# Kernel optimization log

Measured on AMD Instinct MI355X. Metric: run time of the kernel, lower is better.

Reference implementation:

```python
import jax, jax.numpy as jnp
import numpy as np

B, S, D, H = 4, 2048, 512, 8  # batch, seq, input_dim=feature_dim, n_heads


def setup_inputs() -> dict:
    key = jax.random.key(0)
    ks = jax.random.split(key, 12)
    s = 1.0 / np.sqrt(D)
    return {
        "q": jax.random.normal(ks[0], (B, S, D), jnp.float32),
        "k": jax.random.normal(ks[1], (B, S, D), jnp.float32),
        "v": jax.random.normal(ks[2], (B, S, D), jnp.float32),
        "mask": jax.random.randint(ks[3], (B, S), 0, 2, jnp.int32),
        "wq": jax.random.uniform(ks[4], (D, D), jnp.float32, -s, s),
        "bq": jax.random.uniform(ks[5], (D,), jnp.float32, -s, s),
        "wk": jax.random.uniform(ks[6], (D, D), jnp.float32, -s, s),
        "bk": jax.random.uniform(ks[7], (D,), jnp.float32, -s, s),
        "wv": jax.random.uniform(ks[8], (D, D), jnp.float32, -s, s),
        "bv": jax.random.uniform(ks[9], (D,), jnp.float32, -s, s),
        "wd": jax.random.uniform(ks[10], (D, D), jnp.float32, -s, s),
        "bd": jax.random.uniform(ks[11], (D,), jnp.float32, -s, s),
    }


def reference(q, k, v, mask, wq, bq, wk, bk, wv, bv, wd, bd):
    hd = D // H
    # linear projections [B,S,D]
    qp = q @ wq + bq
    kp = k @ wk + bk
    vp = v @ wv + bv
    # split heads -> [B,H,S,hd]
    split = lambda x: x.reshape(B, S, H, hd).transpose(0, 2, 1, 3)
    qh, kh, vh = split(qp), split(kp), split(vp)
    # scaled dot-product attention with additive mask [B,1,1,S]
    scores = jnp.einsum("bhqd,bhkd->bhqk", qh, kh) / np.sqrt(hd)
    scores = scores + mask.astype(scores.dtype)[:, None, None, :] * (-1e9)
    weights = jax.nn.softmax(scores, axis=-1)
    attn = jnp.einsum("bhqk,bhkd->bhqd", weights, vh)
    # merge heads -> [B,S,D], final dense
    attn = attn.transpose(0, 2, 1, 3).reshape(B, S, D)
    return attn @ wd + bd
```

## Files before the change

kernel.cpp:

```cpp
#include <hip/hip_runtime.h>
#include <hip/hip_bf16.h>
#include <cmath>

typedef __bf16 bf16;
typedef __attribute__((ext_vector_type(8))) __bf16 bf16x8;
typedef __attribute__((ext_vector_type(4))) __bf16 bf16x4;
typedef __attribute__((ext_vector_type(4))) float f32x4;

#define LOG2E 1.4426950408889634f

__global__ __launch_bounds__(256)
void prep_w(const float* __restrict__ w0, const float* __restrict__ w1,
            const float* __restrict__ w2, const float* __restrict__ w3,
            bf16* __restrict__ wt)
{
    const float* W = (blockIdx.z == 0) ? w0 : (blockIdx.z == 1) ? w1
                   : (blockIdx.z == 2) ? w2 : w3;
    bf16* WT = wt + (size_t)blockIdx.z * 512 * 512;

    __shared__ bf16 t[64][72];
    const int k0 = blockIdx.x * 64, n0 = blockIdx.y * 64;
    const int tid = threadIdx.x;
    {
        const int row = tid >> 2;
        const int c0 = (tid & 3) * 16;
        const float* src = W + (size_t)(k0 + row) * 512 + n0 + c0;
#pragma unroll
        for (int i = 0; i < 16; i += 4) {
            f32x4 f = *(const f32x4*)(src + i);
            t[c0 + i + 0][row] = (bf16)f[0];
            t[c0 + i + 1][row] = (bf16)f[1];
            t[c0 + i + 2][row] = (bf16)f[2];
            t[c0 + i + 3][row] = (bf16)f[3];
        }
    }
    __syncthreads();
    {
        const int nrow = tid >> 2;
        const int c0 = (tid & 3) * 16;
        bf16* dst = WT + (size_t)(n0 + nrow) * 512 + k0 + c0;
        *(bf16x8*)(dst)     = *(const bf16x8*)&t[nrow][c0];
        *(bf16x8*)(dst + 8) = *(const bf16x8*)&t[nrow][c0 + 8];
    }
}

__global__ __launch_bounds__(256)
void proj_kernel(const float* __restrict__ qin, const float* __restrict__ kin,
                 const float* __restrict__ vin, const bf16* __restrict__ wt,
                 const float* __restrict__ bq, const float* __restrict__ bk,
                 const float* __restrict__ bv, bf16* __restrict__ qp,
                 bf16* __restrict__ kp, bf16* __restrict__ vpT)
{
    const int z = blockIdx.z;
    const float* A    = (z == 0) ? qin : (z == 1) ? kin : vin;
    const bf16* WT    = wt + (size_t)z * 262144;
    const float* bias = (z == 0) ? bq : (z == 1) ? bk : bv;
    const float scale = (z == 0) ? 0.125f * LOG2E : 1.0f;

    const int row0 = blockIdx.x * 64;
    const int col0 = blockIdx.y * 128;
    const int tid = threadIdx.x;
    const int wave = tid >> 6, lane = tid & 63;
    const int wr = wave >> 1, wc = wave & 1;
    const int g = lane >> 4, r = lane & 15;

    __shared__ bf16 As[64][72];
    __shared__ bf16 Bs[128][72];

    const int arow = tid >> 2, ak0 = (tid & 3) * 16;
    const int brow = tid >> 1, bk0 = (tid & 1) * 32;

    f32x4 a0, a1, a2, a3;
    bf16x8 b0, b1, b2, b3;
    {
        const float* asrc = A + (size_t)(row0 + arow) * 512 + ak0;
        a0 = *(const f32x4*)(asrc);     a1 = *(const f32x4*)(asrc + 4);
        a2 = *(const f32x4*)(asrc + 8); a3 = *(const f32x4*)(asrc + 12);
        const bf16* bsrc = WT + (size_t)(col0 + brow) * 512 + bk0;
        b0 = *(const bf16x8*)(bsrc);      b1 = *(const bf16x8*)(bsrc + 8);
        b2 = *(const bf16x8*)(bsrc + 16); b3 = *(const bf16x8*)(bsrc + 24);
    }

    f32x4 acc[2][4] = {};

    for (int kt = 0; kt < 512; kt += 64) {
        {
            bf16x8 v0, v1;
#pragma unroll
            for (int i = 0; i < 4; i++) {
                v0[i] = (bf16)a0[i]; v0[4+i] = (bf16)a1[i];
                v1[i] = (bf16)a2[i]; v1[4+i] = (bf16)a3[i];
            }
            *(bf16x8*)&As[arow][ak0]     = v0;
            *(bf16x8*)&As[arow][ak0 + 8] = v1;
            *(bf16x8*)&Bs[brow][bk0]      = b0;
            *(bf16x8*)&Bs[brow][bk0 +  8] = b1;
            *(bf16x8*)&Bs[brow][bk0 + 16] = b2;
            *(bf16x8*)&Bs[brow][bk0 + 24] = b3;
        }
        __syncthreads();

        if (kt + 64 < 512) {
            const float* asrc = A + (size_t)(row0 + arow) * 512 + kt + 64 + ak0;
            a0 = *(const f32x4*)(asrc);     a1 = *(const f32x4*)(asrc + 4);
            a2 = *(const f32x4*)(asrc + 8); a3 = *(const f32x4*)(asrc + 12);
            const bf16* bsrc = WT + (size_t)(col0 + brow) * 512 + kt + 64 + bk0;
            b0 = *(const bf16x8*)(bsrc);      b1 = *(const bf16x8*)(bsrc + 8);
            b2 = *(const bf16x8*)(bsrc + 16); b3 = *(const bf16x8*)(bsrc + 24);
        }

#pragma unroll
        for (int kk = 0; kk < 64; kk += 32) {
            bf16x8 af[2], bfr[4];
#pragma unroll
            for (int mf = 0; mf < 2; mf++)
                af[mf] = *(const bf16x8*)&As[wr*32 + mf*16 + r][kk + g*8];
#pragma unroll
            for (int nf = 0; nf < 4; nf++)
                bfr[nf] = *(const bf16x8*)&Bs[wc*64 + nf*16 + r][kk + g*8];
#pragma unroll
            for (int mf = 0; mf < 2; mf++)
#pragma unroll
                for (int nf = 0; nf < 4; nf++)
                    acc[mf][nf] = __builtin_amdgcn_mfma_f32_16x16x32_bf16(
                        af[mf], bfr[nf], acc[mf][nf], 0, 0, 0);
        }
        __syncthreads();
    }

#pragma unroll
    for (int mf = 0; mf < 2; mf++) {
#pragma unroll
        for (int nf = 0; nf < 4; nf++) {
            const int rbase = row0 + wr*32 + mf*16 + g*4;
            const int ccol  = col0 + wc*64 + nf*16 + r;
            const float bi = bias[ccol];
            const int h = ccol >> 6, hd = ccol & 63;
            if (z < 2) {
                bf16* C = (z == 0) ? qp : kp;
#pragma unroll
                for (int j = 0; j < 4; j++) {
                    const int rrow = rbase + j;
                    const int b = rrow >> 11, s = rrow & 2047;
                    C[(((size_t)(b*8 + h) * 2048) + s) * 64 + hd] =
                        (bf16)((acc[mf][nf][j] + bi) * scale);
                }
            } else {
                const int b = rbase >> 11, s = rbase & 2047;
                bf16x4 pk;
#pragma unroll
                for (int j = 0; j < 4; j++) pk[j] = (bf16)(acc[mf][nf][j] + bi);
                *(bf16x4*)(vpT + ((size_t)(b*8 + h) * 64 + hd) * 2048 + s) = pk;
            }
        }
    }
}

__global__ __launch_bounds__(256)
void dense_kernel(const bf16* __restrict__ ab, const bf16* __restrict__ WT,
                  const float* __restrict__ bias, float* __restrict__ out)
{
    const int row0 = blockIdx.x * 64;
    const int col0 = blockIdx.y * 128;
    const int tid = threadIdx.x;
    const int wave = tid >> 6, lane = tid & 63;
    const int wr = wave >> 1, wc = wave & 1;
    const int g = lane >> 4, r = lane & 15;

    __shared__ bf16 As[64][72];
    __shared__ bf16 Bs[128][72];

    const int arow = tid >> 2, ak0 = (tid & 3) * 16;
    const int brow = tid >> 1, bk0 = (tid & 1) * 32;

    bf16x8 aR0, aR1, b0, b1, b2, b3;
    {
        const bf16* asrc = ab + (size_t)(row0 + arow) * 512 + ak0;
        aR0 = *(const bf16x8*)(asrc); aR1 = *(const bf16x8*)(asrc + 8);
        const bf16* bsrc = WT + (size_t)(col0 + brow) * 512 + bk0;
        b0 = *(const bf16x8*)(bsrc);      b1 = *(const bf16x8*)(bsrc + 8);
        b2 = *(const bf16x8*)(bsrc + 16); b3 = *(const bf16x8*)(bsrc + 24);
    }

    f32x4 acc[2][4] = {};

    for (int kt = 0; kt < 512; kt += 64) {
        *(bf16x8*)&As[arow][ak0]     = aR0;
        *(bf16x8*)&As[arow][ak0 + 8] = aR1;
        *(bf16x8*)&Bs[brow][bk0]      = b0;
        *(bf16x8*)&Bs[brow][bk0 +  8] = b1;
        *(bf16x8*)&Bs[brow][bk0 + 16] = b2;
        *(bf16x8*)&Bs[brow][bk0 + 24] = b3;
        __syncthreads();

        if (kt + 64 < 512) {
            const bf16* asrc = ab + (size_t)(row0 + arow) * 512 + kt + 64 + ak0;
            aR0 = *(const bf16x8*)(asrc); aR1 = *(const bf16x8*)(asrc + 8);
            const bf16* bsrc = WT + (size_t)(col0 + brow) * 512 + kt + 64 + bk0;
            b0 = *(const bf16x8*)(bsrc);      b1 = *(const bf16x8*)(bsrc + 8);
            b2 = *(const bf16x8*)(bsrc + 16); b3 = *(const bf16x8*)(bsrc + 24);
        }

#pragma unroll
        for (int kk = 0; kk < 64; kk += 32) {
            bf16x8 af[2], bfr[4];
#pragma unroll
            for (int mf = 0; mf < 2; mf++)
                af[mf] = *(const bf16x8*)&As[wr*32 + mf*16 + r][kk + g*8];
#pragma unroll
            for (int nf = 0; nf < 4; nf++)
                bfr[nf] = *(const bf16x8*)&Bs[wc*64 + nf*16 + r][kk + g*8];
#pragma unroll
            for (int mf = 0; mf < 2; mf++)
#pragma unroll
                for (int nf = 0; nf < 4; nf++)
                    acc[mf][nf] = __builtin_amdgcn_mfma_f32_16x16x32_bf16(
                        af[mf], bfr[nf], acc[mf][nf], 0, 0, 0);
        }
        __syncthreads();
    }

#pragma unroll
    for (int mf = 0; mf < 2; mf++) {
#pragma unroll
        for (int nf = 0; nf < 4; nf++) {
            const int rbase = row0 + wr*32 + mf*16 + g*4;
            const int ccol  = col0 + wc*64 + nf*16 + r;
            const float bi = bias[ccol];
#pragma unroll
            for (int j = 0; j < 4; j++)
                out[(size_t)(rbase + j) * 512 + ccol] = acc[mf][nf][j] + bi;
        }
    }
}

__global__ __launch_bounds__(256)
void attn_kernel(const bf16* __restrict__ qp, const bf16* __restrict__ kp,
                 const bf16* __restrict__ vpT, const int* __restrict__ mask,
                 bf16* __restrict__ attn)
{
    const int bh = blockIdx.x;
    const int qt = blockIdx.y;
    const int b = bh >> 3, h = bh & 7;
    const int tid = threadIdx.x;
    const int w = tid >> 6, lane = tid & 63;
    const int g = (lane >> 4) & 3, r = lane & 15;

    __shared__ bf16 QPs[128][72];
    __shared__ bf16 Ks[2][64][72];
    __shared__ bf16 Vt[2][64][72];
    __shared__ __align__(16) float madd2[2048];

    const size_t head_base = (size_t)(b*8 + h) * 2048 * 64;
    const int q0 = qt * 128;
    const bf16* kbase = kp  + head_base;
    const bf16* vbase = vpT + head_base;

    {
        const int4* m4 = (const int4*)(mask + b * 2048);
#pragma unroll
        for (int i = 0; i < 2; i++) {
            const int4 mv = m4[tid*2 + i];
            f32x4 f;
            f[0] = mv.x ? -1.4426950e9f : 0.f;
            f[1] = mv.y ? -1.4426950e9f : 0.f;
            f[2] = mv.z ? -1.4426950e9f : 0.f;
            f[3] = mv.w ? -1.4426950e9f : 0.f;
            *(f32x4*)&madd2[tid*8 + i*4] = f;
        }
    }
    {
        const int row = tid >> 1;
        const int c0 = (tid & 1) * 32;
        const bf16* src = qp + head_base + (size_t)(q0 + row) * 64 + c0;
        *(bf16x8*)&QPs[row][c0]      = *(const bf16x8*)(src);
        *(bf16x8*)&QPs[row][c0 +  8] = *(const bf16x8*)(src + 8);
        *(bf16x8*)&QPs[row][c0 + 16] = *(const bf16x8*)(src + 16);
        *(bf16x8*)&QPs[row][c0 + 24] = *(const bf16x8*)(src + 24);
    }
    bf16x8 qf[2][2];
#pragma unroll
    for (int qs = 0; qs < 2; qs++)
#pragma unroll
        for (int ks = 0; ks < 2; ks++)
            qf[qs][ks] = *(const bf16x8*)&QPs[w*32 + qs*16 + r][ks*32 + g*8];

    const int srow = tid >> 2;
    const int sc0  = (tid & 3) * 16;
    bf16x8 kr0, kr1, vr0, vr1;
    kr0 = *(const bf16x8*)(kbase + (size_t)srow * 64 + sc0);
    kr1 = *(const bf16x8*)(kbase + (size_t)srow * 64 + sc0 + 8);
    vr0 = *(const bf16x8*)(vbase + (size_t)srow * 2048 + sc0);
    vr1 = *(const bf16x8*)(vbase + (size_t)srow * 2048 + sc0 + 8);
    *(bf16x8*)&Ks[0][srow][sc0]     = kr0;
    *(bf16x8*)&Ks[0][srow][sc0 + 8] = kr1;
    *(bf16x8*)&Vt[0][srow][sc0]     = vr0;
    *(bf16x8*)&Vt[0][srow][sc0 + 8] = vr1;

    float m2[2] = {-INFINITY, -INFINITY};
    f32x4 oT[2][4] = {};
    f32x4 lac[2] = {};
    bf16x8 ones;
#pragma unroll
    for (int i = 0; i < 8; i++) ones[i] = (bf16)1.0f;

    int it = 0;
    for (int kt = 0; kt < 2048; kt += 64, it ^= 1) {
        __syncthreads();
        const bool more = (kt + 64) < 2048;
        if (more) {
            kr0 = *(const bf16x8*)(kbase + (size_t)(kt+64+srow)*64 + sc0);
            kr1 = *(const bf16x8*)(kbase + (size_t)(kt+64+srow)*64 + sc0 + 8);
            vr0 = *(const bf16x8*)(vbase + (size_t)srow*2048 + kt+64 + sc0);
            vr1 = *(const bf16x8*)(vbase + (size_t)srow*2048 + kt+64 + sc0 + 8);
        }

        f32x4 sa[2][4] = {};
        __builtin_amdgcn_s_setprio(1);
#pragma unroll
        for (int ks = 0; ks < 2; ks++) {
            bf16x8 kfrag[4];
#pragma unroll
            for (int kf = 0; kf < 4; kf++)
                kfrag[kf] = *(const bf16x8*)&Ks[it][kf*16 + r][ks*32 + g*8];
#pragma unroll
            for (int qs = 0; qs < 2; qs++)
#pragma unroll
                for (int kf = 0; kf < 4; kf++)
                    sa[qs][kf] = __builtin_amdgcn_mfma_f32_16x16x32_bf16(
                        kfrag[kf], qf[qs][ks], sa[qs][kf], 0, 0, 0);
        }
        __builtin_amdgcn_s_setprio(0);

        f32x4 ma[4];
#pragma unroll
        for (int kf = 0; kf < 4; kf++)
            ma[kf] = *(const f32x4*)&madd2[kt + kf*16 + g*4];

#pragma unroll
        for (int qs = 0; qs < 2; qs++) {
            f32x4 sv[4];
            float mx = -INFINITY;
#pragma unroll
            for (int kf = 0; kf < 4; kf++) {
                sv[kf] = sa[qs][kf] + ma[kf];
                mx = fmaxf(mx, fmaxf(fmaxf(sv[kf][0], sv[kf][1]),
                                     fmaxf(sv[kf][2], sv[kf][3])));
            }
            if (!__all(mx <= m2[qs] + 11.54f)) {
                mx = fmaxf(mx, __shfl_xor(mx, 16, 64));
                mx = fmaxf(mx, __shfl_xor(mx, 32, 64));
                const float mn = fmaxf(m2[qs], mx);
                const float corr = __builtin_amdgcn_exp2f(m2[qs] - mn);
#pragma unroll
                for (int vf = 0; vf < 4; vf++) oT[qs][vf] *= corr;
                lac[qs] *= corr;
                m2[qs] = mn;
            }
#pragma unroll
            for (int kf = 0; kf < 4; kf++) {
                bf16x4 pkk;
#pragma unroll
                for (int j = 0; j < 4; j++)
                    pkk[j] = (bf16)__builtin_amdgcn_exp2f(sv[kf][j] - m2[qs]);
                *(bf16x4*)&QPs[w*32 + qs*16 + r][kf*16 + g*4] = pkk;
            }
        }

        __builtin_amdgcn_s_setprio(1);
#pragma unroll
        for (int ks = 0; ks < 2; ks++) {
            bf16x8 vfrag[4];
#pragma unroll
            for (int vf = 0; vf < 4; vf++)
                vfrag[vf] = *(const bf16x8*)&Vt[it][vf*16 + r][ks*32 + g*8];
#pragma unroll
            for (int qs = 0; qs < 2; qs++) {
                const bf16x8 pf = *(const bf16x8*)&QPs[w*32 + qs*16 + r][ks*32 + g*8];
                lac[qs] = __builtin_amdgcn_mfma_f32_16x16x32_bf16(
                    ones, pf, lac[qs], 0, 0, 0);
#pragma unroll
                for (int vf = 0; vf < 4; vf++)
                    oT[qs][vf] = __builtin_amdgcn_mfma_f32_16x16x32_bf16(
                        vfrag[vf], pf, oT[qs][vf], 0, 0, 0);
            }
        }
        __builtin_amdgcn_s_setprio(0);

        if (more) {
            *(bf16x8*)&Ks[it^1][srow][sc0]     = kr0;
            *(bf16x8*)&Ks[it^1][srow][sc0 + 8] = kr1;
            *(bf16x8*)&Vt[it^1][srow][sc0]     = vr0;
            *(bf16x8*)&Vt[it^1][srow][sc0 + 8] = vr1;
        }
    }

#pragma unroll
    for (int qs = 0; qs < 2; qs++) {
        const float inv = 1.0f / lac[qs][0];
        const int s = q0 + w*32 + qs*16 + r;
        bf16* dst = attn + ((size_t)(b*2048) + s) * 512 + h*64 + g*4;
#pragma unroll
        for (int vf = 0; vf < 4; vf++) {
            bf16x4 ov;
#pragma unroll
            for (int j = 0; j < 4; j++) ov[j] = (bf16)(oT[qs][vf][j] * inv);
            *(bf16x4*)(dst + vf*16) = ov;
        }
    }
}

extern "C" void kernel_launch(void* const* d_in, const int* in_sizes, int n_in,
                              void* d_out, int out_size, void* d_ws, size_t ws_size,
                              hipStream_t stream)
{
    const float* q    = (const float*)d_in[0];
    const float* k    = (const float*)d_in[1];
    const float* v    = (const float*)d_in[2];
    const int*   mask = (const int*)  d_in[3];
    const float* wq   = (const float*)d_in[4];
    const float* bq   = (const float*)d_in[5];
    const float* wk   = (const float*)d_in[6];
    const float* bk   = (const float*)d_in[7];
    const float* wv   = (const float*)d_in[8];
    const float* bv   = (const float*)d_in[9];
    const float* wd   = (const float*)d_in[10];
    const float* bd   = (const float*)d_in[11];
    float* out = (float*)d_out;

    const size_t NELEM = (size_t)4 * 2048 * 512;
    bf16* qp  = (bf16*)d_ws;
    bf16* kp  = qp + NELEM;
    bf16* vpT = kp + NELEM;
    bf16* ab  = vpT + NELEM;
    bf16* wt  = ab + NELEM;

    prep_w<<<dim3(8, 8, 4), dim3(256), 0, stream>>>(wq, wk, wv, wd, wt);

    proj_kernel<<<dim3(128, 4, 3), dim3(256), 0, stream>>>(
        q, k, v, wt, bq, bk, bv, qp, kp, vpT);

    attn_kernel<<<dim3(32, 16), dim3(256), 0, stream>>>(qp, kp, vpT, mask, ab);

    dense_kernel<<<dim3(128, 4), dim3(256), 0, stream>>>(
        ab, wt + 3*262144, bd, out);
}
```

Measured before the change: 113.6 us.

## Use 32x32x16 MFMA in attention with register-resident P via permlane32 swap

Rewrites the attention inner loop to use 32x32x16 bf16 MFMAs, so each wave handles 32 query rows with one accumulator per 32-key half. The P tile no longer round-trips through LDS: probabilities are packed to bf16 in registers and rearranged with v_permlane32_swap to form the B operand for the PV MFMA. The row sum is now an explicit VALU sum plus a cross-half shuffle instead of an extra MFMA against a ones vector. Q fragments load straight from global memory, which drops the QPs shared buffer and its synchronization. The cost is more inline asm and a layout that depends on the exact fragment mapping being correct.

```diff
diff --git a/kernel.cpp b/kernel.cpp
--- a/kernel.cpp
+++ b/kernel.cpp
@@ -6,6 +6,7 @@
 typedef __attribute__((ext_vector_type(8))) __bf16 bf16x8;
 typedef __attribute__((ext_vector_type(4))) __bf16 bf16x4;
 typedef __attribute__((ext_vector_type(4))) float f32x4;
+typedef __attribute__((ext_vector_type(16))) float f32x16;
 
 #define LOG2E 1.4426950408889634f
 
@@ -244,9 +245,9 @@
     const int b = bh >> 3, h = bh & 7;
     const int tid = threadIdx.x;
     const int w = tid >> 6, lane = tid & 63;
-    const int g = (lane >> 4) & 3, r = lane & 15;
-
-    __shared__ bf16 QPs[128][72];
+    const int c = lane & 31;
+    const int hi = lane >> 5;
+
     __shared__ bf16 Ks[2][64][72];
     __shared__ bf16 Vt[2][64][72];
     __shared__ __align__(16) float madd2[2048];
@@ -269,21 +270,14 @@
             *(f32x4*)&madd2[tid*8 + i*4] = f;
         }
     }
-    {
-        const int row = tid >> 1;
-        const int c0 = (tid & 1) * 32;
-        const bf16* src = qp + head_base + (size_t)(q0 + row) * 64 + c0;
-        *(bf16x8*)&QPs[row][c0]      = *(const bf16x8*)(src);
-        *(bf16x8*)&QPs[row][c0 +  8] = *(const bf16x8*)(src + 8);
-        *(bf16x8*)&QPs[row][c0 + 16] = *(const bf16x8*)(src + 16);
-        *(bf16x8*)&QPs[row][c0 + 24] = *(const bf16x8*)(src + 24);
-    }
-    bf16x8 qf[2][2];
-#pragma unroll
-    for (int qs = 0; qs < 2; qs++)
-#pragma unroll
-        for (int ks = 0; ks < 2; ks++)
-            qf[qs][ks] = *(const bf16x8*)&QPs[w*32 + qs*16 + r][ks*32 + g*8];
+
+    bf16x8 qf[4];
+    {
+        const bf16* qsrc = qp + head_base + (size_t)(q0 + w*32 + c) * 64 + hi*8;
+#pragma unroll
+        for (int kstep = 0; kstep < 4; kstep++)
+            qf[kstep] = *(const bf16x8*)(qsrc + kstep*16);
+    }
 
     const int srow = tid >> 2;
     const int sc0  = (tid & 3) * 16;
@@ -297,12 +291,8 @@
     *(bf16x8*)&Vt[0][srow][sc0]     = vr0;
     *(bf16x8*)&Vt[0][srow][sc0 + 8] = vr1;
 
-    float m2[2] = {-INFINITY, -INFINITY};
-    f32x4 oT[2][4] = {};
-    f32x4 lac[2] = {};
-    bf16x8 ones;
-#pragma unroll
-    for (int i = 0; i < 8; i++) ones[i] = (bf16)1.0f;
+    float m_run = -INFINITY, l_run = 0.f;
+    f32x16 oT0 = {}, oT1 = {};
 
     int it = 0;
     for (int kt = 0; kt < 2048; kt += 64, it ^= 1) {
@@ -315,74 +305,75 @@
             vr1 = *(const bf16x8*)(vbase + (size_t)srow*2048 + kt+64 + sc0 + 8);
         }
 
-        f32x4 sa[2][4] = {};
+        f32x16 sa0 = {}, sa1 = {};
         __builtin_amdgcn_s_setprio(1);
 #pragma unroll
-        for (int ks = 0; ks < 2; ks++) {
-            bf16x8 kfrag[4];
-#pragma unroll
-            for (int kf = 0; kf < 4; kf++)
-                kfrag[kf] = *(const bf16x8*)&Ks[it][kf*16 + r][ks*32 + g*8];
-#pragma unroll
-            for (int qs = 0; qs < 2; qs++)
-#pragma unroll
-                for (int kf = 0; kf < 4; kf++)
-                    sa[qs][kf] = __builtin_amdgcn_mfma_f32_16x16x32_bf16(
-                        kfrag[kf], qf[qs][ks], sa[qs][kf], 0, 0, 0);
+        for (int kstep = 0; kstep < 4; kstep++) {
+            const bf16x8 k0 = *(const bf16x8*)&Ks[it][c][kstep*16 + hi*8];
+            const bf16x8 k1 = *(const bf16x8*)&Ks[it][32 + c][kstep*16 + hi*8];
+            sa0 = __builtin_amdgcn_mfma_f32_32x32x16_bf16(k0, qf[kstep], sa0, 0, 0, 0);
+            sa1 = __builtin_amdgcn_mfma_f32_32x32x16_bf16(k1, qf[kstep], sa1, 0, 0, 0);
         }
         __builtin_amdgcn_s_setprio(0);
 
-        f32x4 ma[4];
-#pragma unroll
-        for (int kf = 0; kf < 4; kf++)
-            ma[kf] = *(const f32x4*)&madd2[kt + kf*16 + g*4];
-
-#pragma unroll
-        for (int qs = 0; qs < 2; qs++) {
-            f32x4 sv[4];
-            float mx = -INFINITY;
-#pragma unroll
-            for (int kf = 0; kf < 4; kf++) {
-                sv[kf] = sa[qs][kf] + ma[kf];
-                mx = fmaxf(mx, fmaxf(fmaxf(sv[kf][0], sv[kf][1]),
-                                     fmaxf(sv[kf][2], sv[kf][3])));
+        float mx = -INFINITY;
+#pragma unroll
+        for (int t = 0; t < 4; t++) {
+            const f32x4 ma0 = *(const f32x4*)&madd2[kt +      t*8 + hi*4];
+            const f32x4 ma1 = *(const f32x4*)&madd2[kt + 32 + t*8 + hi*4];
+#pragma unroll
+            for (int j = 0; j < 4; j++) {
+                sa0[t*4+j] += ma0[j];
+                sa1[t*4+j] += ma1[j];
+                mx = fmaxf(mx, fmaxf(sa0[t*4+j], sa1[t*4+j]));
             }
-            if (!__all(mx <= m2[qs] + 11.54f)) {
-                mx = fmaxf(mx, __shfl_xor(mx, 16, 64));
-                mx = fmaxf(mx, __shfl_xor(mx, 32, 64));
-                const float mn = fmaxf(m2[qs], mx);
-                const float corr = __builtin_amdgcn_exp2f(m2[qs] - mn);
-#pragma unroll
-                for (int vf = 0; vf < 4; vf++) oT[qs][vf] *= corr;
-                lac[qs] *= corr;
-                m2[qs] = mn;
-            }
-#pragma unroll
-            for (int kf = 0; kf < 4; kf++) {
-                bf16x4 pkk;
-#pragma unroll
-                for (int j = 0; j < 4; j++)
-                    pkk[j] = (bf16)__builtin_amdgcn_exp2f(sv[kf][j] - m2[qs]);
-                *(bf16x4*)&QPs[w*32 + qs*16 + r][kf*16 + g*4] = pkk;
-            }
-        }
+        }
+        if (!__all(mx <= m_run + 11.54f)) {
+            mx = fmaxf(mx, __shfl_xor(mx, 32, 64));
+            const float mn = fmaxf(m_run, mx);
+            const float corr = __builtin_amdgcn_exp2f(m_run - mn);
+            oT0 *= corr; oT1 *= corr; l_run *= corr;
+            m_run = mn;
+        }
+
+        float psum = 0.f;
+        unsigned int z[2][4][2];
+#pragma unroll
+        for (int t = 0; t < 4; t++) {
+            float p0 = __builtin_amdgcn_exp2f(sa0[t*4+0] - m_run);
+            float p1 = __builtin_amdgcn_exp2f(sa0[t*4+1] - m_run);
+            float p2 = __builtin_amdgcn_exp2f(sa0[t*4+2] - m_run);
+            float p3 = __builtin_amdgcn_exp2f(sa0[t*4+3] - m_run);
+            asm("v_cvt_pk_bf16_f32 %0, %1, %2" : "=v"(z[0][t][0]) : "v"(p0), "v"(p1));
+            asm("v_cvt_pk_bf16_f32 %0, %1, %2" : "=v"(z[0][t][1]) : "v"(p2), "v"(p3));
+            psum += (p0 + p1) + (p2 + p3);
+            float q4 = __builtin_amdgcn_exp2f(sa1[t*4+0] - m_run);
+            float q5 = __builtin_amdgcn_exp2f(sa1[t*4+1] - m_run);
+            float q6 = __builtin_amdgcn_exp2f(sa1[t*4+2] - m_run);
+            float q7 = __builtin_amdgcn_exp2f(sa1[t*4+3] - m_run);
+            asm("v_cvt_pk_bf16_f32 %0, %1, %2" : "=v"(z[1][t][0]) : "v"(q4), "v"(q5));
+            asm("v_cvt_pk_bf16_f32 %0, %1, %2" : "=v"(z[1][t][1]) : "v"(q6), "v"(q7));
+            psum += (q4 + q5) + (q6 + q7);
+        }
+        psum += __shfl_xor(psum, 32, 64);
+        l_run += psum;
 
         __builtin_amdgcn_s_setprio(1);
 #pragma unroll
-        for (int ks = 0; ks < 2; ks++) {
-            bf16x8 vfrag[4];
-#pragma unroll
-            for (int vf = 0; vf < 4; vf++)
-                vfrag[vf] = *(const bf16x8*)&Vt[it][vf*16 + r][ks*32 + g*8];
-#pragma unroll
-            for (int qs = 0; qs < 2; qs++) {
-                const bf16x8 pf = *(const bf16x8*)&QPs[w*32 + qs*16 + r][ks*32 + g*8];
-                lac[qs] = __builtin_amdgcn_mfma_f32_16x16x32_bf16(
-                    ones, pf, lac[qs], 0, 0, 0);
-#pragma unroll
-                for (int vf = 0; vf < 4; vf++)
-                    oT[qs][vf] = __builtin_amdgcn_mfma_f32_16x16x32_bf16(
-                        vfrag[vf], pf, oT[qs][vf], 0, 0, 0);
+        for (int kg = 0; kg < 2; kg++) {
+#pragma unroll
+            for (int ksl = 0; ksl < 2; ksl++) {
+                unsigned int a0 = z[kg][2*ksl][0], a1 = z[kg][2*ksl][1];
+                unsigned int b0 = z[kg][2*ksl+1][0], b1 = z[kg][2*ksl+1][1];
+                asm volatile("v_permlane32_swap_b32 %0, %1" : "+v"(a0), "+v"(b0));
+                asm volatile("v_permlane32_swap_b32 %0, %1" : "+v"(a1), "+v"(b1));
+                union { unsigned int u[4]; bf16x8 v; } pf;
+                pf.u[0] = a0; pf.u[1] = a1; pf.u[2] = b0; pf.u[3] = b1;
+                const int kcol = (kg*2 + ksl)*16 + hi*8;
+                const bf16x8 v0 = *(const bf16x8*)&Vt[it][c][kcol];
+                const bf16x8 v1 = *(const bf16x8*)&Vt[it][32 + c][kcol];
+                oT0 = __builtin_amdgcn_mfma_f32_32x32x16_bf16(v0, pf.v, oT0, 0, 0, 0);
+                oT1 = __builtin_amdgcn_mfma_f32_32x32x16_bf16(v1, pf.v, oT1, 0, 0, 0);
             }
         }
         __builtin_amdgcn_s_setprio(0);
@@ -395,18 +386,19 @@
         }
     }
 
-#pragma unroll
-    for (int qs = 0; qs < 2; qs++) {
-        const float inv = 1.0f / lac[qs][0];
-        const int s = q0 + w*32 + qs*16 + r;
-        bf16* dst = attn + ((size_t)(b*2048) + s) * 512 + h*64 + g*4;
-#pragma unroll
-        for (int vf = 0; vf < 4; vf++) {
-            bf16x4 ov;
-#pragma unroll
-            for (int j = 0; j < 4; j++) ov[j] = (bf16)(oT[qs][vf][j] * inv);
-            *(bf16x4*)(dst + vf*16) = ov;
-        }
+    const float inv = 1.0f / l_run;
+    const int s = q0 + w*32 + c;
+    bf16* dst = attn + ((size_t)(b*2048) + s) * 512 + h*64;
+#pragma unroll
+    for (int t = 0; t < 4; t++) {
+        bf16x4 o0, o1;
+#pragma unroll
+        for (int j = 0; j < 4; j++) {
+            o0[j] = (bf16)(oT0[t*4+j] * inv);
+            o1[j] = (bf16)(oT1[t*4+j] * inv);
+        }
+        *(bf16x4*)(dst +      t*8 + hi*4) = o0;
+        *(bf16x4*)(dst + 32 + t*8 + hi*4) = o1;
     }
 }
 
```

Result: faster. 105.8 us (-6.9%).
